# Optimization experiments

Measured on AMD Instinct MI355X. Metric: run time of the kernel, lower is better.

Reference implementation:

```python
import jax, jax.numpy as jnp
from jax import lax
import numpy as np

DIM = 384
HEADS = 8
B, H, W = 8, 128, 128
_DN = ('NCHW', 'OIHW', 'NCHW')


def setup_inputs() -> dict:
    key = jax.random.key(0)
    ks = jax.random.split(key, 8)
    x = jax.random.normal(ks[0], (B, DIM, H, W), jnp.float32)
    qkv_w = jax.random.normal(ks[1], (3 * DIM, DIM, 1, 1), jnp.float32) * 0.02
    qkv_b = jax.random.normal(ks[2], (3 * DIM,), jnp.float32) * 0.02
    dw_w = jax.random.normal(ks[3], (3 * DIM, 1, 3, 3), jnp.float32) * 0.02
    dw_b = jax.random.normal(ks[4], (3 * DIM,), jnp.float32) * 0.02
    proj_w = jax.random.normal(ks[5], (DIM, DIM, 1, 1), jnp.float32) * 0.02
    proj_b = jax.random.normal(ks[6], (DIM,), jnp.float32) * 0.02
    temperature = jnp.ones((HEADS, 1, 1), jnp.float32)
    return {"x": x, "qkv_w": qkv_w, "qkv_b": qkv_b, "dw_w": dw_w,
            "dw_b": dw_b, "proj_w": proj_w, "proj_b": proj_b,
            "temperature": temperature}


def _l2norm(t, eps=1e-12):
    # F.normalize(t, dim=-1): divide by max(||t||_2, eps)
    n = jnp.sqrt(jnp.sum(t * t, axis=-1, keepdims=True))
    return t / jnp.maximum(n, eps)


def reference(x, qkv_w, qkv_b, dw_w, dw_b, proj_w, proj_b, temperature):
    b, C, h, w = x.shape
    heads = HEADS
    c = C // heads
    hw = h * w
    # 1x1 pointwise qkv conv
    qkv = lax.conv_general_dilated(x, qkv_w, (1, 1), 'VALID',
                                   dimension_numbers=_DN) + qkv_b[None, :, None, None]
    # 3x3 depthwise conv, padding=1
    qkv = lax.conv_general_dilated(qkv, dw_w, (1, 1), ((1, 1), (1, 1)),
                                   feature_group_count=3 * C,
                                   dimension_numbers=_DN) + dw_b[None, :, None, None]
    q, k, v = jnp.split(qkv, 3, axis=1)
    # b (head c) h w -> b head c (h w)
    q = q.reshape(b, heads, c, hw)
    k = k.reshape(b, heads, c, hw)
    v = v.reshape(b, heads, c, hw)
    q = _l2norm(q)
    k = _l2norm(k)
    # processor scales q by temperature*sqrt(hw); SDPA divides by sqrt(hw):
    # net logits = temperature * q_n @ k_n^T  (CxC channel attention per head)
    temp = temperature.reshape(1, heads, 1, 1)
    logits = jnp.einsum('bhcn,bhdn->bhcd', q * temp, k)
    attn = jax.nn.softmax(logits, axis=-1)
    out = jnp.einsum('bhcd,bhdn->bhcn', attn, v)  # [b, heads, c, hw]
    out = out.reshape(b, C, h, w)
    return lax.conv_general_dilated(out, proj_w, (1, 1), 'VALID',
                                    dimension_numbers=_DN) + proj_b[None, :, None, None]
```

## Files before the change

kernel.cpp:

```cpp
#include <hip/hip_runtime.h>
#include <hip/hip_bf16.h>
#include <cstdint>


#define BATCH 8
#define DIM 384
#define HEADS 8
#define CH 48
#define HW 16384
#define C3 1152
#define MPAD1 1280
#define WPAD 512

typedef __attribute__((ext_vector_type(8))) short bf16x8;
typedef __attribute__((ext_vector_type(8))) unsigned short u16x8;
typedef __attribute__((ext_vector_type(4))) float f32x4;

__device__ __forceinline__ float b2f(ushort b) {
  union { float f; unsigned u; } x; x.u = ((unsigned)b) << 16; return x.f;
}
__device__ __forceinline__ ushort f2b(float f) {
  union { float f; unsigned u; } x; x.f = f;
  unsigned r = x.u + 0x7fffu + ((x.u >> 16) & 1u);
  return (ushort)(r >> 16);
}

__device__ __forceinline__ void async16(const ushort* g, ushort* l) {
  __builtin_amdgcn_global_load_lds(
      (const __attribute__((address_space(1))) unsigned int*)(unsigned long long)(uintptr_t)g,
      (__attribute__((address_space(3))) unsigned int*)(unsigned int)(uintptr_t)l,
      16, 0, 0);
}

__global__ __launch_bounds__(256) void cast_w(const float* __restrict__ s,
                                              ushort* __restrict__ d, int n) {
  int i = (blockIdx.x * 256 + threadIdx.x) * 4;
  if (i + 3 < n) {
    float4 v = *(const float4*)(s + i);
    ushort4 o = make_ushort4(f2b(v.x), f2b(v.y), f2b(v.z), f2b(v.w));
    *(ushort4*)(d + i) = o;
  }
}

template <typename SrcT, int OUT_BF16>
__global__ __launch_bounds__(512, 1) void gemm_px2(
    const ushort* __restrict__ A, const SrcT* __restrict__ src,
    const float* __restrict__ bias, void* __restrict__ Cout,
    int Mpad, int Mreal, long Asb, long Ssb, long Csb) {
  constexpr int K = DIM;
  int zb = blockIdx.y;
  int px0 = blockIdx.x * 128;
  const ushort* Ab = A + (size_t)zb * Asb;
  const SrcT* Sb = src + (size_t)zb * Ssb;
  __shared__ __align__(16) ushort Bs[128 * 384];
  __shared__ __align__(16) ushort As[2][256 * 64];
  int tid = threadIdx.x, lane = tid & 63, wid = tid >> 6;
  int wm = wid >> 1, wn = wid & 1;
  int fr = lane & 15, fs = lane >> 4;

  {
    int pix = tid & 127;
    int cg = tid >> 7;
#pragma unroll
    for (int rr = 0; rr < 12; ++rr) {
      int c8 = cg + rr * 4;
      u16x8 pk;
#pragma unroll
      for (int j = 0; j < 8; ++j) {
        int c = c8 * 8 + j;
        if constexpr (sizeof(SrcT) == 4)
          pk[j] = f2b(((const float*)Sb)[(size_t)c * HW + px0 + pix]);
        else
          pk[j] = ((const ushort*)Sb)[(size_t)c * HW + px0 + pix];
      }
      *(u16x8*)&Bs[pix * 384 + ((c8 ^ (pix & 7)) << 3)] = pk;
    }
  }

  auto stageA = [&](int buf, int mt, int k0) {
#pragma unroll
    for (int q = 0; q < 4; ++q) {
      int r = q * 64 + wid * 8 + (lane >> 3);
      int col = ((lane & 7) ^ (r & 7)) * 8;
      async16(Ab + (size_t)(mt * 256 + r) * K + k0 + col,
              &As[buf][(q * 64 + wid * 8) * 64]);
    }
  };

  f32x4 acc[4][4];
  auto compute = [&](int buf, int t) {
#pragma unroll
    for (int kk = 0; kk < 2; ++kk) {
      bf16x8 af[4], bv[4];
#pragma unroll
      for (int m = 0; m < 4; ++m) {
        int R = wm * 64 + m * 16 + fr;
        int slot = kk * 4 + fs;
        af[m] = *(const bf16x8*)&As[buf][R * 64 + ((slot ^ (R & 7)) << 3)];
      }
#pragma unroll
      for (int n = 0; n < 4; ++n) {
        int P = wn * 64 + n * 16 + fr;
        int gslot = t * 8 + kk * 4 + fs;
        bv[n] = *(const bf16x8*)&Bs[P * 384 + ((gslot ^ (P & 7)) << 3)];
      }
#pragma unroll
      for (int m = 0; m < 4; ++m)
#pragma unroll
        for (int n = 0; n < 4; ++n)
          acc[m][n] = __builtin_amdgcn_mfma_f32_16x16x32_bf16(af[m], bv[n], acc[m][n], 0, 0, 0);
    }
  };

  const int MT = Mpad >> 8;
  stageA(0, 0, 0);
  __syncthreads();

  for (int mt = 0; mt < MT; ++mt) {
    f32x4 zero = {0.f, 0.f, 0.f, 0.f};
#pragma unroll
    for (int m = 0; m < 4; ++m)
#pragma unroll
      for (int n = 0; n < 4; ++n) acc[m][n] = zero;
#pragma unroll
    for (int t = 0; t < 5; ++t) {
      stageA((t + 1) & 1, mt, (t + 1) * 64);
      __builtin_amdgcn_s_setprio(1);
      compute(t & 1, t);
      __builtin_amdgcn_s_setprio(0);
      __syncthreads();
    }
    if (mt + 1 < MT) stageA(0, mt + 1, 0);
    __builtin_amdgcn_s_setprio(1);
    compute(1, 5);
    __builtin_amdgcn_s_setprio(0);
#pragma unroll
    for (int m = 0; m < 4; ++m)
#pragma unroll
      for (int j = 0; j < 4; ++j) {
        int gr = mt * 256 + wm * 64 + m * 16 + fs * 4 + j;
        if (gr < Mreal) {
          float bz = bias[gr];
#pragma unroll
          for (int n = 0; n < 4; ++n) {
            int gc = px0 + wn * 64 + n * 16 + fr;
            float v = acc[m][n][j] + bz;
            if constexpr (OUT_BF16)
              ((ushort*)Cout)[(size_t)zb * Csb + (size_t)gr * HW + gc] = f2b(v);
            else
              ((float*)Cout)[(size_t)zb * Csb + (size_t)gr * HW + gc] = v;
          }
        }
      }
    __syncthreads();
  }
}

__global__ __launch_bounds__(256) void dwconv(
    const ushort* __restrict__ in, const float* __restrict__ w9,
    const float* __restrict__ b9, ushort* __restrict__ out,
    float* __restrict__ sq) {
  int ch = blockIdx.x;
  int b = blockIdx.y;
  const size_t plane = ((size_t)b * C3 + ch) * HW;
  int tid = threadIdx.x, lane = tid & 63;
  int rg = tid >> 4, cg = tid & 15;
  int r0 = rg * 8, c0 = cg * 8;

  float w[9];
#pragma unroll
  for (int i = 0; i < 9; ++i) w[i] = w9[ch * 9 + i];
  float bias = b9[ch];

  float a0[8], a1[8];
#pragma unroll
  for (int c = 0; c < 8; ++c) { a0[c] = 0.f; a1[c] = 0.f; }
  float ss = 0.f;

#pragma unroll
  for (int it = 0; it < 10; ++it) {
    int r = r0 - 1 + it;
    float x[8];
    if ((unsigned)r < 128u) {
      u16x8 raw = *(const u16x8*)(in + plane + (size_t)r * 128 + c0);
#pragma unroll
      for (int c = 0; c < 8; ++c) x[c] = b2f(raw[c]);
    } else {
#pragma unroll
      for (int c = 0; c < 8; ++c) x[c] = 0.f;
    }
    float xl = __shfl(x[7], lane - 1);
    float xr = __shfl(x[0], lane + 1);
    if (cg == 0) xl = 0.f;
    if (cg == 15) xr = 0.f;

    float h0[8], h1[8], h2[8];
#pragma unroll
    for (int c = 0; c < 8; ++c) {
      float l = (c == 0) ? xl : x[c - 1];
      float rt = (c == 7) ? xr : x[c + 1];
      h0[c] = w[0] * l + w[1] * x[c] + w[2] * rt;
      h1[c] = w[3] * l + w[4] * x[c] + w[5] * rt;
      h2[c] = w[6] * l + w[7] * x[c] + w[8] * rt;
    }
    if (it >= 2) {
      int R = r - 1;
      u16x8 pk;
#pragma unroll
      for (int c = 0; c < 8; ++c) {
        float o = a0[c] + h2[c] + bias;
        ss += o * o;
        pk[c] = f2b(o);
      }
      *(u16x8*)(out + plane + (size_t)R * 128 + c0) = pk;
    }
#pragma unroll
    for (int c = 0; c < 8; ++c) { a0[c] = a1[c] + h1[c]; a1[c] = h0[c]; }
  }

  if (ch < 2 * DIM) {
#pragma unroll
    for (int off = 32; off; off >>= 1) ss += __shfl_down(ss, off, 64);
    if (lane == 0) atomicAdd(&sq[b * 2 * DIM + ch], ss);
  }
}

__global__ __launch_bounds__(256) void gram(const ushort* __restrict__ qkvd,
                                            float* __restrict__ G) {
  int chunk = blockIdx.x;
  int bh = blockIdx.y;
  int b = bh >> 3, h = bh & 7;
  int tid = threadIdx.x, lane = tid & 63, wid = tid >> 6;
  const ushort* qbase = qkvd + ((size_t)b * C3 + h * CH) * HW;
  const ushort* kbase = qbase + (size_t)DIM * HW;
  int pix0 = chunk * 1024 + wid * 256;
  int fr = lane & 15, fk = (lane >> 4) * 8;
  f32x4 zero = {0.f, 0.f, 0.f, 0.f};
  f32x4 acc[3][3];
#pragma unroll
  for (int i = 0; i < 3; ++i)
#pragma unroll
    for (int j = 0; j < 3; ++j) acc[i][j] = zero;
#pragma unroll
  for (int it = 0; it < 8; ++it) {
    int pix = pix0 + it * 32 + fk;
    bf16x8 aq[3], bk[3];
#pragma unroll
    for (int mi = 0; mi < 3; ++mi)
      aq[mi] = *(const bf16x8*)(qbase + (size_t)(mi * 16 + fr) * HW + pix);
#pragma unroll
    for (int ni = 0; ni < 3; ++ni)
      bk[ni] = *(const bf16x8*)(kbase + (size_t)(ni * 16 + fr) * HW + pix);
#pragma unroll
    for (int mi = 0; mi < 3; ++mi)
#pragma unroll
      for (int ni = 0; ni < 3; ++ni)
        acc[mi][ni] = __builtin_amdgcn_mfma_f32_16x16x32_bf16(aq[mi], bk[ni], acc[mi][ni], 0, 0, 0);
  }
  __shared__ float gs[CH * CH];
  for (int i = tid; i < CH * CH; i += 256) gs[i] = 0.f;
  __syncthreads();
  int crow = (lane >> 4) * 4, ccol = lane & 15;
#pragma unroll
  for (int mi = 0; mi < 3; ++mi)
#pragma unroll
    for (int ni = 0; ni < 3; ++ni)
#pragma unroll
      for (int j = 0; j < 4; ++j)
        atomicAdd(&gs[(mi * 16 + crow + j) * CH + ni * 16 + ccol], acc[mi][ni][j]);
  __syncthreads();
  float* Gp = G + (size_t)bh * CH * CH;
  for (int i = tid; i < CH * CH; i += 256) atomicAdd(&Gp[i], gs[i]);
}

__global__ void softmax_k(const float* __restrict__ G, const float* __restrict__ sq,
                          const float* __restrict__ temp, float* __restrict__ attn) {
  int bh = blockIdx.x, b = bh >> 3, h = bh & 7;
  int lane = threadIdx.x;
  __shared__ float inq[CH], ink[CH];
  if (lane < CH) {
    inq[lane] = 1.f / fmaxf(sqrtf(sq[b * 2 * DIM + h * CH + lane]), 1e-12f);
    ink[lane] = 1.f / fmaxf(sqrtf(sq[b * 2 * DIM + DIM + h * CH + lane]), 1e-12f);
  }
  __syncthreads();
  if (lane < CH) {
    float t = temp[h] * inq[lane];
    const float* g = G + (size_t)bh * CH * CH + lane * CH;
    float v[CH];
    float mx = -1e30f;
#pragma unroll
    for (int d = 0; d < CH; ++d) { v[d] = t * g[d] * ink[d]; mx = fmaxf(mx, v[d]); }
    float s = 0.f;
#pragma unroll
    for (int d = 0; d < CH; ++d) { v[d] = expf(v[d] - mx); s += v[d]; }
    float inv = 1.f / s;
    float* a = attn + (size_t)bh * CH * CH + lane * CH;
#pragma unroll
    for (int d = 0; d < CH; ++d) a[d] = v[d] * inv;
  }
}

__global__ __launch_bounds__(384) void weff_k(const float* __restrict__ pw,
                                              const float* __restrict__ attn,
                                              ushort* __restrict__ weff) {
  int dg = threadIdx.x;
  int p = blockIdx.x;
  int b = blockIdx.y;
  int h = dg / CH, d = dg - h * CH;
  const float* a = attn + (((size_t)b * HEADS + h) * CH) * CH + d;
  const float* wrow = pw + (size_t)p * DIM + h * CH;
  float s = 0.f;
#pragma unroll
  for (int c = 0; c < CH; ++c) s += wrow[c] * a[c * CH];
  weff[((size_t)b * WPAD + p) * DIM + dg] = f2b(s);
}

extern "C" void kernel_launch(void* const* d_in, const int* in_sizes, int n_in,
                              void* d_out, int out_size, void* d_ws, size_t ws_size,
                              hipStream_t stream) {
  const float* x = (const float*)d_in[0];
  const float* qkv_w = (const float*)d_in[1];
  const float* qkv_b = (const float*)d_in[2];
  const float* dw_w = (const float*)d_in[3];
  const float* dw_b = (const float*)d_in[4];
  const float* proj_w = (const float*)d_in[5];
  const float* proj_b = (const float*)d_in[6];
  const float* temp = (const float*)d_in[7];

  const size_t SZ_C1 = (size_t)BATCH * C3 * HW * 2;
  const size_t SZ_WQB = (size_t)MPAD1 * DIM * 2;
  const size_t SZ_SQ = (size_t)BATCH * 2 * DIM * 4;
  const size_t SZ_G = (size_t)BATCH * HEADS * CH * CH * 4;
  const size_t SZ_WEFF = (size_t)BATCH * WPAD * DIM * 2;

  const size_t OFF_C1 = 0;
  const size_t OFF_QKVD = OFF_C1 + SZ_C1;
  const size_t OFF_WQB = OFF_QKVD + SZ_C1;
  const size_t OFF_SQ = OFF_WQB + SZ_WQB;
  const size_t OFF_G = OFF_SQ + SZ_SQ;
  const size_t OFF_ATTN = OFF_G + SZ_G;
  const size_t OFF_WEFF = OFF_ATTN + SZ_G;
  const size_t TOTAL = OFF_WEFF + SZ_WEFF;
  if (ws_size < TOTAL) return;

  char* ws = (char*)d_ws;
  ushort* c1 = (ushort*)(ws + OFF_C1);
  ushort* qkvd = (ushort*)(ws + OFF_QKVD);
  ushort* wqb = (ushort*)(ws + OFF_WQB);
  float* sq = (float*)(ws + OFF_SQ);
  float* G = (float*)(ws + OFF_G);
  float* attn = (float*)(ws + OFF_ATTN);
  ushort* weff = (ushort*)(ws + OFF_WEFF);

  hipMemsetAsync(ws + OFF_SQ, 0, SZ_SQ + SZ_G, stream);

  cast_w<<<(C3 * DIM) / 1024, 256, 0, stream>>>(qkv_w, wqb, C3 * DIM);
  gemm_px2<float, 1><<<dim3(HW / 128, BATCH), 512, 0, stream>>>(
      wqb, x, qkv_b, (void*)c1, MPAD1, C3, 0L, (long)DIM * HW, (long)C3 * HW);
  dwconv<<<dim3(C3, BATCH), 256, 0, stream>>>(c1, dw_w, dw_b, qkvd, sq);
  gram<<<dim3(16, BATCH * HEADS), 256, 0, stream>>>(qkvd, G);
  softmax_k<<<BATCH * HEADS, 64, 0, stream>>>(G, sq, temp, attn);
  weff_k<<<dim3(DIM, BATCH), 384, 0, stream>>>(proj_w, attn, weff);
  gemm_px2<ushort, 0><<<dim3(HW / 128, BATCH), 512, 0, stream>>>(
      weff, qkvd + (size_t)2 * DIM * HW, proj_b, d_out, WPAD, DIM,
      (long)WPAD * DIM, (long)C3 * HW, (long)DIM * HW);
}
```

Measured before the change: 576.1 us.

## Make pointwise GEMMs weight-stationary in registers with double-buffered pixel panels

Restructures both 1x1-conv GEMMs so each wave keeps its 32 weight rows for the full K=384 in registers, instead of streaming weight tiles through LDS with async loads. Each block now covers one 256-row M slice and walks several 64-pixel panels. The next panel is prefetched into registers and written into a second LDS buffer while the current panel feeds the MFMAs. This drops the per-k-step weight staging and most barriers. The cost is that the activation input is now re-read once per M slice (5x for the qkv GEMM), plus more register pressure and fewer, larger blocks.

After: 1.057 ms. 1.83x slower.

```diff
diff --git a/kernel.cpp b/kernel.cpp
--- a/kernel.cpp
+++ b/kernel.cpp
@@ -25,13 +25,6 @@
   return (ushort)(r >> 16);
 }
 
-__device__ __forceinline__ void async16(const ushort* g, ushort* l) {
-  __builtin_amdgcn_global_load_lds(
-      (const __attribute__((address_space(1))) unsigned int*)(unsigned long long)(uintptr_t)g,
-      (__attribute__((address_space(3))) unsigned int*)(unsigned int)(uintptr_t)l,
-      16, 0, 0);
-}
-
 __global__ __launch_bounds__(256) void cast_w(const float* __restrict__ s,
                                               ushort* __restrict__ d, int n) {
   int i = (blockIdx.x * 256 + threadIdx.x) * 4;
@@ -43,27 +36,33 @@
 }
 
 template <typename SrcT, int OUT_BF16>
-__global__ __launch_bounds__(512, 1) void gemm_px2(
+__global__ __launch_bounds__(512, 1) void gemm_ws(
     const ushort* __restrict__ A, const SrcT* __restrict__ src,
     const float* __restrict__ bias, void* __restrict__ Cout,
-    int Mpad, int Mreal, long Asb, long Ssb, long Csb) {
-  constexpr int K = DIM;
-  int zb = blockIdx.y;
-  int px0 = blockIdx.x * 128;
+    int Mreal, long Asb, long Ssb, long Csb, int npanels) {
+  int zb = blockIdx.z;
+  int m0 = blockIdx.y * 256;
+  int pxbase = blockIdx.x * npanels * 64;
   const ushort* Ab = A + (size_t)zb * Asb;
   const SrcT* Sb = src + (size_t)zb * Ssb;
-  __shared__ __align__(16) ushort Bs[128 * 384];
-  __shared__ __align__(16) ushort As[2][256 * 64];
+  __shared__ __align__(16) ushort Bs[2][64 * 384];
   int tid = threadIdx.x, lane = tid & 63, wid = tid >> 6;
-  int wm = wid >> 1, wn = wid & 1;
   int fr = lane & 15, fs = lane >> 4;
+  int wrow = m0 + wid * 32;
+  int pix = tid & 63, cg = tid >> 6;
+
+  bf16x8 af0[12], af1[12];
+#pragma unroll
+  for (int s = 0; s < 12; ++s) {
+    af0[s] = *(const bf16x8*)(Ab + (size_t)(wrow + fr) * 384 + s * 32 + fs * 8);
+    af1[s] = *(const bf16x8*)(Ab + (size_t)(wrow + 16 + fr) * 384 + s * 32 + fs * 8);
+  }
 
   {
-    int pix = tid & 127;
-    int cg = tid >> 7;
-#pragma unroll
-    for (int rr = 0; rr < 12; ++rr) {
-      int c8 = cg + rr * 4;
+    int px0 = pxbase;
+#pragma unroll
+    for (int rr = 0; rr < 6; ++rr) {
+      int c8 = cg + rr * 8;
       u16x8 pk;
 #pragma unroll
       for (int j = 0; j < 8; ++j) {
@@ -73,77 +72,76 @@
         else
           pk[j] = ((const ushort*)Sb)[(size_t)c * HW + px0 + pix];
       }
-      *(u16x8*)&Bs[pix * 384 + ((c8 ^ (pix & 7)) << 3)] = pk;
-    }
-  }
-
-  auto stageA = [&](int buf, int mt, int k0) {
-#pragma unroll
-    for (int q = 0; q < 4; ++q) {
-      int r = q * 64 + wid * 8 + (lane >> 3);
-      int col = ((lane & 7) ^ (r & 7)) * 8;
-      async16(Ab + (size_t)(mt * 256 + r) * K + k0 + col,
-              &As[buf][(q * 64 + wid * 8) * 64]);
-    }
-  };
-
-  f32x4 acc[4][4];
-  auto compute = [&](int buf, int t) {
-#pragma unroll
-    for (int kk = 0; kk < 2; ++kk) {
-      bf16x8 af[4], bv[4];
-#pragma unroll
-      for (int m = 0; m < 4; ++m) {
-        int R = wm * 64 + m * 16 + fr;
-        int slot = kk * 4 + fs;
-        af[m] = *(const bf16x8*)&As[buf][R * 64 + ((slot ^ (R & 7)) << 3)];
-      }
+      *(u16x8*)&Bs[0][pix * 384 + ((c8 ^ (pix & 7)) << 3)] = pk;
+    }
+  }
+  __syncthreads();
+
+  int cur = 0;
+#pragma unroll 1
+  for (int p = 0; p < npanels; ++p) {
+    int px0 = pxbase + p * 64;
+    bool more = (p + 1 < npanels);
+    float lf[48];
+    ushort lu[48];
+    if (more) {
+      int px1 = px0 + 64;
+#pragma unroll
+      for (int rr = 0; rr < 6; ++rr)
+#pragma unroll
+        for (int j = 0; j < 8; ++j) {
+          int c = (cg + rr * 8) * 8 + j;
+          if constexpr (sizeof(SrcT) == 4)
+            lf[rr * 8 + j] = ((const float*)Sb)[(size_t)c * HW + px1 + pix];
+          else
+            lu[rr * 8 + j] = ((const ushort*)Sb)[(size_t)c * HW + px1 + pix];
+        }
+    }
+    f32x4 acc[2][4];
+    f32x4 zero = {0.f, 0.f, 0.f, 0.f};
+#pragma unroll
+    for (int m = 0; m < 2; ++m)
+#pragma unroll
+      for (int n = 0; n < 4; ++n) acc[m][n] = zero;
+    __builtin_amdgcn_s_setprio(1);
+#pragma unroll
+    for (int s = 0; s < 12; ++s) {
+      bf16x8 bv[4];
 #pragma unroll
       for (int n = 0; n < 4; ++n) {
-        int P = wn * 64 + n * 16 + fr;
-        int gslot = t * 8 + kk * 4 + fs;
-        bv[n] = *(const bf16x8*)&Bs[P * 384 + ((gslot ^ (P & 7)) << 3)];
-      }
-#pragma unroll
-      for (int m = 0; m < 4; ++m)
-#pragma unroll
-        for (int n = 0; n < 4; ++n)
-          acc[m][n] = __builtin_amdgcn_mfma_f32_16x16x32_bf16(af[m], bv[n], acc[m][n], 0, 0, 0);
-    }
-  };
-
-  const int MT = Mpad >> 8;
-  stageA(0, 0, 0);
-  __syncthreads();
-
-  for (int mt = 0; mt < MT; ++mt) {
-    f32x4 zero = {0.f, 0.f, 0.f, 0.f};
-#pragma unroll
-    for (int m = 0; m < 4; ++m)
-#pragma unroll
-      for (int n = 0; n < 4; ++n) acc[m][n] = zero;
-#pragma unroll
-    for (int t = 0; t < 5; ++t) {
-      stageA((t + 1) & 1, mt, (t + 1) * 64);
-      __builtin_amdgcn_s_setprio(1);
-      compute(t & 1, t);
-      __builtin_amdgcn_s_setprio(0);
-      __syncthreads();
-    }
-    if (mt + 1 < MT) stageA(0, mt + 1, 0);
-    __builtin_amdgcn_s_setprio(1);
-    compute(1, 5);
+        int P = n * 16 + fr;
+        bv[n] = *(const bf16x8*)&Bs[cur][P * 384 + (((s * 4 + fs) ^ (P & 7)) << 3)];
+      }
+#pragma unroll
+      for (int n = 0; n < 4; ++n) {
+        acc[0][n] = __builtin_amdgcn_mfma_f32_16x16x32_bf16(af0[s], bv[n], acc[0][n], 0, 0, 0);
+        acc[1][n] = __builtin_amdgcn_mfma_f32_16x16x32_bf16(af1[s], bv[n], acc[1][n], 0, 0, 0);
+      }
+    }
     __builtin_amdgcn_s_setprio(0);
-#pragma unroll
-    for (int m = 0; m < 4; ++m)
+    if (more) {
+#pragma unroll
+      for (int rr = 0; rr < 6; ++rr) {
+        int c8 = cg + rr * 8;
+        u16x8 pk;
+#pragma unroll
+        for (int j = 0; j < 8; ++j) {
+          if constexpr (sizeof(SrcT) == 4) pk[j] = f2b(lf[rr * 8 + j]);
+          else pk[j] = lu[rr * 8 + j];
+        }
+        *(u16x8*)&Bs[cur ^ 1][pix * 384 + ((c8 ^ (pix & 7)) << 3)] = pk;
+      }
+    }
+#pragma unroll
+    for (int m = 0; m < 2; ++m)
 #pragma unroll
       for (int j = 0; j < 4; ++j) {
-        int gr = mt * 256 + wm * 64 + m * 16 + fs * 4 + j;
+        int gr = wrow + m * 16 + fs * 4 + j;
         if (gr < Mreal) {
           float bz = bias[gr];
 #pragma unroll
           for (int n = 0; n < 4; ++n) {
-            int gc = px0 + wn * 64 + n * 16 + fr;
+            int gc = px0 + n * 16 + fr;
             float v = acc[m][n][j] + bz;
             if constexpr (OUT_BF16)
               ((ushort*)Cout)[(size_t)zb * Csb + (size_t)gr * HW + gc] = f2b(v);
@@ -153,6 +151,7 @@
         }
       }
     __syncthreads();
+    cur ^= 1;
   }
 }
 
@@ -355,13 +354,13 @@
   hipMemsetAsync(ws + OFF_SQ, 0, SZ_SQ + SZ_G, stream);
 
   cast_w<<<(C3 * DIM) / 1024, 256, 0, stream>>>(qkv_w, wqb, C3 * DIM);
-  gemm_px2<float, 1><<<dim3(HW / 128, BATCH), 512, 0, stream>>>(
-      wqb, x, qkv_b, (void*)c1, MPAD1, C3, 0L, (long)DIM * HW, (long)C3 * HW);
+  gemm_ws<float, 1><<<dim3(32, 5, BATCH), 512, 0, stream>>>(
+      wqb, x, qkv_b, (void*)c1, C3, 0L, (long)DIM * HW, (long)C3 * HW, 8);
   dwconv<<<dim3(C3, BATCH), 256, 0, stream>>>(c1, dw_w, dw_b, qkvd, sq);
   gram<<<dim3(16, BATCH * HEADS), 256, 0, stream>>>(qkvd, G);
   softmax_k<<<BATCH * HEADS, 64, 0, stream>>>(G, sq, temp, attn);
   weff_k<<<dim3(DIM, BATCH), 384, 0, stream>>>(proj_w, attn, weff);
-  gemm_px2<ushort, 0><<<dim3(HW / 128, BATCH), 512, 0, stream>>>(
-      weff, qkvd + (size_t)2 * DIM * HW, proj_b, d_out, WPAD, DIM,
-      (long)WPAD * DIM, (long)C3 * HW, (long)DIM * HW);
-}
+  gemm_ws<ushort, 0><<<dim3(16, 2, BATCH), 512, 0, stream>>>(
+      weff, qkvd + (size_t)2 * DIM * HW, proj_b, d_out, DIM,
+      (long)WPAD * DIM, (long)C3 * HW, (long)DIM * HW, 16);
+}
```

## Shrink GEMM pixel tile to 64 and run two single-buffered blocks per CU

Applied to the files above, without the earlier changes.

The pointwise GEMM kernel now uses 256-thread blocks over 64-pixel tiles, with each wave owning 64 rows of the A tile. A is single-buffered with a barrier before and after each K step, where before it was double-buffered with prefetch. Smaller LDS (about 80KB) lets two blocks share a CU, so one block's compute can hide the other's loads instead of relying on in-block prefetch. In exchange, A-weight traffic per pixel doubles and each K step waits on its own load with no intra-block overlap.

Result: slower. 627.1 us (+8.8%).

```diff
diff --git a/kernel.cpp b/kernel.cpp
--- a/kernel.cpp
+++ b/kernel.cpp
@@ -43,24 +43,23 @@
 }
 
 template <typename SrcT, int OUT_BF16>
-__global__ __launch_bounds__(512, 1) void gemm_px2(
+__global__ __launch_bounds__(256, 2) void gemm_fat(
     const ushort* __restrict__ A, const SrcT* __restrict__ src,
     const float* __restrict__ bias, void* __restrict__ Cout,
     int Mpad, int Mreal, long Asb, long Ssb, long Csb) {
   constexpr int K = DIM;
   int zb = blockIdx.y;
-  int px0 = blockIdx.x * 128;
+  int px0 = blockIdx.x * 64;
   const ushort* Ab = A + (size_t)zb * Asb;
   const SrcT* Sb = src + (size_t)zb * Ssb;
-  __shared__ __align__(16) ushort Bs[128 * 384];
-  __shared__ __align__(16) ushort As[2][256 * 64];
+  __shared__ __align__(16) ushort Bs[64 * 384];
+  __shared__ __align__(16) ushort As[256 * 64];
   int tid = threadIdx.x, lane = tid & 63, wid = tid >> 6;
-  int wm = wid >> 1, wn = wid & 1;
   int fr = lane & 15, fs = lane >> 4;
 
   {
-    int pix = tid & 127;
-    int cg = tid >> 7;
+    int pix = tid & 63;
+    int cg = tid >> 6;
 #pragma unroll
     for (int rr = 0; rr < 12; ++rr) {
       int c8 = cg + rr * 4;
@@ -77,30 +76,30 @@
     }
   }
 
-  auto stageA = [&](int buf, int mt, int k0) {
-#pragma unroll
-    for (int q = 0; q < 4; ++q) {
-      int r = q * 64 + wid * 8 + (lane >> 3);
+  auto stageA = [&](int mt, int k0) {
+#pragma unroll
+    for (int q = 0; q < 8; ++q) {
+      int r = q * 32 + wid * 8 + (lane >> 3);
       int col = ((lane & 7) ^ (r & 7)) * 8;
       async16(Ab + (size_t)(mt * 256 + r) * K + k0 + col,
-              &As[buf][(q * 64 + wid * 8) * 64]);
+              &As[(q * 32 + wid * 8) * 64]);
     }
   };
 
   f32x4 acc[4][4];
-  auto compute = [&](int buf, int t) {
+  auto compute = [&](int t) {
 #pragma unroll
     for (int kk = 0; kk < 2; ++kk) {
       bf16x8 af[4], bv[4];
 #pragma unroll
       for (int m = 0; m < 4; ++m) {
-        int R = wm * 64 + m * 16 + fr;
+        int R = wid * 64 + m * 16 + fr;
         int slot = kk * 4 + fs;
-        af[m] = *(const bf16x8*)&As[buf][R * 64 + ((slot ^ (R & 7)) << 3)];
+        af[m] = *(const bf16x8*)&As[R * 64 + ((slot ^ (R & 7)) << 3)];
       }
 #pragma unroll
       for (int n = 0; n < 4; ++n) {
-        int P = wn * 64 + n * 16 + fr;
+        int P = n * 16 + fr;
         int gslot = t * 8 + kk * 4 + fs;
         bv[n] = *(const bf16x8*)&Bs[P * 384 + ((gslot ^ (P & 7)) << 3)];
       }
@@ -113,9 +112,6 @@
   };
 
   const int MT = Mpad >> 8;
-  stageA(0, 0, 0);
-  __syncthreads();
-
   for (int mt = 0; mt < MT; ++mt) {
     f32x4 zero = {0.f, 0.f, 0.f, 0.f};
 #pragma unroll
@@ -123,27 +119,24 @@
 #pragma unroll
       for (int n = 0; n < 4; ++n) acc[m][n] = zero;
 #pragma unroll
-    for (int t = 0; t < 5; ++t) {
-      stageA((t + 1) & 1, mt, (t + 1) * 64);
+    for (int t = 0; t < 6; ++t) {
+      stageA(mt, t * 64);
+      __syncthreads();
       __builtin_amdgcn_s_setprio(1);
-      compute(t & 1, t);
+      compute(t);
       __builtin_amdgcn_s_setprio(0);
       __syncthreads();
     }
-    if (mt + 1 < MT) stageA(0, mt + 1, 0);
-    __builtin_amdgcn_s_setprio(1);
-    compute(1, 5);
-    __builtin_amdgcn_s_setprio(0);
 #pragma unroll
     for (int m = 0; m < 4; ++m)
 #pragma unroll
       for (int j = 0; j < 4; ++j) {
-        int gr = mt * 256 + wm * 64 + m * 16 + fs * 4 + j;
+        int gr = mt * 256 + wid * 64 + m * 16 + fs * 4 + j;
         if (gr < Mreal) {
           float bz = bias[gr];
 #pragma unroll
           for (int n = 0; n < 4; ++n) {
-            int gc = px0 + wn * 64 + n * 16 + fr;
+            int gc = px0 + n * 16 + fr;
             float v = acc[m][n][j] + bz;
             if constexpr (OUT_BF16)
               ((ushort*)Cout)[(size_t)zb * Csb + (size_t)gr * HW + gc] = f2b(v);
@@ -152,7 +145,6 @@
           }
         }
       }
-    __syncthreads();
   }
 }
 
@@ -355,13 +347,13 @@
   hipMemsetAsync(ws + OFF_SQ, 0, SZ_SQ + SZ_G, stream);
 
   cast_w<<<(C3 * DIM) / 1024, 256, 0, stream>>>(qkv_w, wqb, C3 * DIM);
-  gemm_px2<float, 1><<<dim3(HW / 128, BATCH), 512, 0, stream>>>(
+  gemm_fat<float, 1><<<dim3(HW / 64, BATCH), 256, 0, stream>>>(
       wqb, x, qkv_b, (void*)c1, MPAD1, C3, 0L, (long)DIM * HW, (long)C3 * HW);
   dwconv<<<dim3(C3, BATCH), 256, 0, stream>>>(c1, dw_w, dw_b, qkvd, sq);
   gram<<<dim3(16, BATCH * HEADS), 256, 0, stream>>>(qkvd, G);
   softmax_k<<<BATCH * HEADS, 64, 0, stream>>>(G, sq, temp, attn);
   weff_k<<<dim3(DIM, BATCH), 384, 0, stream>>>(proj_w, attn, weff);
-  gemm_px2<ushort, 0><<<dim3(HW / 128, BATCH), 512, 0, stream>>>(
+  gemm_fat<ushort, 0><<<dim3(HW / 64, BATCH), 256, 0, stream>>>(
       weff, qkvd + (size_t)2 * DIM * HW, proj_b, d_out, WPAD, DIM,
       (long)WPAD * DIM, (long)C3 * HW, (long)DIM * HW);
 }
```
